# Optimization experiments

Measured on AMD Instinct MI355X. Metric: run time of the kernel, lower is better.

The kernel has to match this reference:

```python
import jax, jax.numpy as jnp
import numpy as np
import math

D_MODEL = 1024
D_INNER = 2048
N_HEADS = 8
D_STATE = 64
D_CONV = 4
CHUNK = 64
HEAD_DIM = D_INNER // N_HEADS
EPS = 1.1920929e-07  # torch RMSNorm default eps = finfo(fp32).eps


def _rms(x, g):
    return x * jax.lax.rsqrt(jnp.mean(x * x, axis=-1, keepdims=True) + EPS) * g


def setup_inputs() -> dict:
    key = jax.random.key(0)
    ks = jax.random.split(key, 8)
    B, S = 32, 256
    proj_out = 2 * D_INNER + 2 * N_HEADS * D_STATE + N_HEADS  # 5128
    s = 0.02
    lambdas = [0.999, 0.995, 0.99, 0.98, 0.95, 0.9, 0.8, 0.7]
    A_log = jnp.log(jnp.asarray([-math.log(l) for l in lambdas], jnp.float32))
    return {
        "hidden": jax.random.normal(ks[0], (B, S, D_MODEL), jnp.float32),
        "W_in": jax.random.normal(ks[1], (proj_out, D_MODEL), jnp.float32) * s,
        "conv_w": jax.random.normal(ks[2], (D_INNER, 1, D_CONV), jnp.float32) * 0.2,
        "conv_b": jax.random.normal(ks[3], (D_INNER,), jnp.float32) * 0.02,
        "W_dt": jax.random.normal(ks[4], (D_INNER, N_HEADS), jnp.float32) * 0.1,
        "b_dt": jax.random.normal(ks[5], (D_INNER,), jnp.float32) * 0.1,
        "A_log": A_log,
        "D": jnp.ones((N_HEADS,), jnp.float32),
        "W_out": jax.random.normal(ks[6], (D_MODEL, D_INNER), jnp.float32) * s,
        "g_in": jnp.ones((D_MODEL,), jnp.float32),
        "g_out": jnp.ones((D_INNER,), jnp.float32),
    }


def reference(hidden, W_in, conv_w, conv_b, W_dt, b_dt, A_log, D, W_out, g_in, g_out):
    B, S, _ = hidden.shape
    residual = hidden
    h = _rms(hidden, g_in)
    proj = h @ W_in.T  # [B,S,5128]
    o1, o2 = D_INNER, 2 * D_INNER
    o3 = o2 + N_HEADS * D_STATE
    o4 = o3 + N_HEADS * D_STATE
    z = proj[..., :o1]
    x = proj[..., o1:o2]
    Bf = proj[..., o2:o3]
    Cf = proj[..., o3:o4]
    dt_raw = proj[..., o4:]
    # causal depthwise conv1d (pad left d_conv-1, trim to S)
    xt = jnp.transpose(x, (0, 2, 1))  # [B, d_inner, S]
    xc = jax.lax.conv_general_dilated(
        xt, conv_w, (1,), [(D_CONV - 1, 0)],
        feature_group_count=D_INNER, dimension_numbers=("NCH", "OIH", "NCH"))
    x = jax.nn.silu(jnp.transpose(xc + conv_b[None, :, None], (0, 2, 1)))
    # dt: project 8 -> d_inner then mean over head_dim -> per-head dt
    dt = dt_raw @ W_dt.T + b_dt  # [B,S,d_inner]
    dt_h = jax.nn.softplus(dt.reshape(B, S, N_HEADS, HEAD_DIM).mean(-1))  # non-TTT path (S<384)
    Bs = Bf.reshape(B, S, N_HEADS, D_STATE)
    Cs = Cf.reshape(B, S, N_HEADS, D_STATE)
    x_h = x.reshape(B, S, N_HEADS, HEAD_DIM)
    # chunked SSD scan
    A = -jnp.exp(A_log)  # [H]
    nC, L = S // CHUNK, CHUNK
    xck = x_h.reshape(B, nC, L, N_HEADS, HEAD_DIM)
    Bck = Bs.reshape(B, nC, L, N_HEADS, D_STATE)
    Cck = Cs.reshape(B, nC, L, N_HEADS, D_STATE)
    logA = dt_h.reshape(B, nC, L, N_HEADS) * A  # [B,c,L,H]
    lcs = jnp.cumsum(logA, axis=2)
    lcs_t = jnp.transpose(lcs, (0, 1, 3, 2))  # [B,c,H,L]
    tril = jnp.tril(jnp.ones((L, L), bool))
    M = jnp.where(tril, jnp.exp(lcs_t[..., :, None] - lcs_t[..., None, :]), 0.0)  # [B,c,H,L,L]
    # intra-chunk: sum_{s<=l,n} C[l,n] M[l,s] B[s,n] x[s,d]
    G = jnp.einsum("bclhn,bcshn->bchls", Cck, Bck)
    intra = jnp.einsum("bchls,bcshd->bclhd", G * M, xck)
    # per-chunk state contributions and decays
    Mlast = jnp.exp(lcs_t[..., -1:] - lcs_t)  # [B,c,H,L] decay from step s to chunk end
    states = jnp.einsum("bchs,bcshn,bcshd->bchdn", Mlast, Bck, xck)  # [B,c,H,hD,N]
    tdec = jnp.exp(lcs[:, :, -1, :])  # [B,c,H]
    def step(hst, inp):
        td, st = inp
        return td[..., None, None] * hst + st, hst
    init = jnp.zeros((B, N_HEADS, HEAD_DIM, D_STATE), x.dtype)
    _, h0 = jax.lax.scan(step, init, (jnp.moveaxis(tdec, 1, 0), jnp.moveaxis(states, 1, 0)))
    # inter-chunk: decay(l) * C[l] . h_start
    inter = jnp.exp(lcs)[..., None] * jnp.einsum("bclhn,cbhdn->bclhd", Cck, h0)
    y = (intra + inter).reshape(B, S, N_HEADS, HEAD_DIM) + x_h * D[None, None, :, None]
    y = y.reshape(B, S, D_INNER) * jax.nn.silu(z)
    y = _rms(y, g_out)
    return residual + y @ W_out.T
```

## Files before the change

kernel.cpp:

```cpp
#include <hip/hip_runtime.h>
#include <hip/hip_bf16.h>
#include <math.h>

typedef __hip_bfloat16 bf16;
typedef __attribute__((ext_vector_type(8))) short short8;
typedef __attribute__((ext_vector_type(4))) float f32x4;

#define AS1 __attribute__((address_space(1)))
#define AS3 __attribute__((address_space(3)))

#define D_MODEL 1024
#define D_INNER 2048
#define N_HEADS 8
#define D_STATE 64
#define CHUNK 64
#define HEAD_DIM 256
#define NCHUNK 4
#define BATCH 32
#define SEQ 256
#define ROWS (BATCH*SEQ)
#define PROJ_N 5128
#define PROJ_NPAD 5248
#define O1 D_INNER
#define O2 (2*D_INNER)
#define O3 (O2 + N_HEADS*D_STATE)
#define O4 (O3 + N_HEADS*D_STATE)
#define EPSF 1.1920929e-07f

__device__ __forceinline__ float silu_f(float x){ return x / (1.0f + expf(-x)); }
__device__ __forceinline__ float b2f(bf16 v){ return __bfloat162float(v); }
__device__ __forceinline__ bf16  f2b(float v){ return __float2bfloat16(v); }
__device__ __forceinline__ short f2s(float v){ bf16 b = __float2bfloat16(v); union{bf16 b; short s;} u; u.b=b; return u.s; }
__device__ __forceinline__ float s2f(short v){ union{short s; bf16 b;} u; u.s=v; return __bfloat162float(u.b); }

__device__ __forceinline__ void gl16(const void* g, void* l){
    __builtin_amdgcn_global_load_lds((const AS1 void*)g, (AS3 void*)l, 16, 0, 0);
}

__device__ __forceinline__ float block_sum_256(float v){
    __shared__ float sm[4];
    #pragma unroll
    for (int o = 32; o > 0; o >>= 1) v += __shfl_down(v, o, 64);
    int lane = threadIdx.x & 63, w = threadIdx.x >> 6;
    if (lane == 0) sm[w] = v;
    __syncthreads();
    return sm[0] + sm[1] + sm[2] + sm[3];
}

__global__ __launch_bounds__(256) void k_rms_in(const float* __restrict__ x,
                                                const float* __restrict__ g,
                                                bf16* __restrict__ out){
    int row = blockIdx.x, t = threadIdx.x;
    const float4* xr = (const float4*)(x + (size_t)row * D_MODEL);
    float4 v = xr[t];
    float ss = v.x*v.x + v.y*v.y + v.z*v.z + v.w*v.w;
    ss = block_sum_256(ss);
    float sc = rsqrtf(ss * (1.0f/(float)D_MODEL) + EPSF);
    float4 gv = ((const float4*)g)[t];
    union { ushort4 u; bf16 b[4]; } o;
    o.b[0] = f2b(v.x*sc*gv.x); o.b[1] = f2b(v.y*sc*gv.y);
    o.b[2] = f2b(v.z*sc*gv.z); o.b[3] = f2b(v.w*sc*gv.w);
    ((ushort4*)(out + (size_t)row * D_MODEL))[t] = o.u;
}

__global__ __launch_bounds__(256) void k_cvt_pad(const float* __restrict__ in,
                                                 bf16* __restrict__ out,
                                                 int n_in, int n_out){
    int i = (blockIdx.x * 256 + threadIdx.x) * 4;
    if (i >= n_out) return;
    union { ushort4 u; bf16 b[4]; } o;
    if (i + 3 < n_in){
        float4 v = *(const float4*)(in + i);
        o.b[0]=f2b(v.x); o.b[1]=f2b(v.y); o.b[2]=f2b(v.z); o.b[3]=f2b(v.w);
    } else {
        #pragma unroll
        for (int j = 0; j < 4; j++) o.b[j] = f2b((i+j < n_in) ? in[i+j] : 0.f);
    }
    *(ushort4*)(out + i) = o.u;
}


__device__ __forceinline__ short8 ld32(const short* base, int row, int g){
    int sr = row >> 1;
    int e8 = (((row & 1) << 2) | g) ^ (sr & 7);
    return *(const short8*)(base + sr*64 + e8*8);
}

__device__ __forceinline__ void stage_j(const bf16* __restrict__ Ag,
                                        const bf16* __restrict__ Bg,
                                        int K, size_t bm, size_t bn, int t,
                                        short* buf, int j){
    const int tid = threadIdx.x;
    const int wid = tid >> 6;
    int cidx = j*256 + tid;
    int srow = cidx >> 3, s8 = cidx & 7;
    int eff = s8 ^ (srow & 7);
    int grow = srow*2 + (eff >> 2);
    int gcol = t*32 + (eff & 3)*8;
    const bf16* src = (grow < 128)
        ? Ag + (bm + grow) * (size_t)K + gcol
        : Bg + (bn + grow - 128) * (size_t)K + gcol;
    gl16(src, buf + (size_t)(j*256 + wid*64)*8);
}

__device__ __forceinline__ void gemm_ring3(const bf16* __restrict__ Ag,
                                           const bf16* __restrict__ Bg,
                                           int K, size_t bm, size_t bn,
                                           short* lds, f32x4 (&acc)[4][4]){
    constexpr int TILE = 256*32;
    const int NT = K >> 5;
    const int lane = threadIdx.x & 63;
    const int wid = threadIdx.x >> 6;
    const int wm = wid >> 1, wn = wid & 1;
    const int fr = lane & 15, g = lane >> 4;

    #pragma unroll
    for (int j = 0; j < 4; j++) stage_j(Ag, Bg, K, bm, bn, 0, lds, j);
    #pragma unroll
    for (int j = 0; j < 4; j++) stage_j(Ag, Bg, K, bm, bn, 1, lds + TILE, j);
    asm volatile("s_waitcnt vmcnt(4)" ::: "memory");
    __builtin_amdgcn_sched_barrier(0);
    __builtin_amdgcn_s_barrier();
    __builtin_amdgcn_sched_barrier(0);

    int cur = 0;
    for (int t = 0; t < NT; t++){
        short* buf = lds + cur*TILE;
        int stgi = cur + 2; if (stgi >= 3) stgi -= 3;
        short* stg = lds + stgi*TILE;
        short8 a[4], b[4];
        #pragma unroll
        for (int m = 0; m < 4; m++) a[m] = ld32(buf, wm*64 + m*16 + fr, g);
        #pragma unroll
        for (int n = 0; n < 4; n++) b[n] = ld32(buf, 128 + wn*64 + n*16 + fr, g);
        if (t + 2 < NT){
            #pragma unroll
            for (int j = 0; j < 4; j++) stage_j(Ag, Bg, K, bm, bn, t+2, stg, j);
        }
        __builtin_amdgcn_s_setprio(1);
        #pragma unroll
        for (int m = 0; m < 4; m++)
            #pragma unroll
            for (int n = 0; n < 4; n++)
                acc[m][n] = __builtin_amdgcn_mfma_f32_16x16x32_bf16(a[m], b[n], acc[m][n], 0, 0, 0);
        __builtin_amdgcn_s_setprio(0);
        __builtin_amdgcn_sched_barrier(0);
        if (t + 2 < NT)      asm volatile("s_waitcnt vmcnt(4)" ::: "memory");
        else if (t + 1 < NT) asm volatile("s_waitcnt vmcnt(0)" ::: "memory");
        __builtin_amdgcn_sched_barrier(0);
        __builtin_amdgcn_s_barrier();
        __builtin_amdgcn_sched_barrier(0);
        cur = cur + 1 == 3 ? 0 : cur + 1;
    }
}

__global__ __launch_bounds__(256, 3) void k_gemm1_r3(const bf16* __restrict__ A,
                                                     const bf16* __restrict__ B,
                                                     bf16* __restrict__ z,
                                                     bf16* __restrict__ xp,
                                                     bf16* __restrict__ Bc,
                                                     bf16* __restrict__ Cc,
                                                     float* __restrict__ dtr){
    extern __shared__ short lds[];
    int wg = (blockIdx.x & 7)*328 + (blockIdx.x >> 3);
    size_t bm = (size_t)(wg / 41) * 128;
    size_t bn = (size_t)(wg % 41) * 128;
    f32x4 acc[4][4] = {};
    gemm_ring3(A, B, D_MODEL, bm, bn, lds, acc);
    const int lane = threadIdx.x & 63;
    const int wid = threadIdx.x >> 6;
    const int wm = wid >> 1, wn = wid & 1;
    int cr = (lane >> 4)*4, cc = lane & 15;
    #pragma unroll
    for (int m = 0; m < 4; m++){
        size_t r0 = bm + wm*64 + m*16 + cr;
        #pragma unroll
        for (int n = 0; n < 4; n++){
            int c = (int)bn + wn*64 + n*16 + cc;
            #pragma unroll
            for (int j = 0; j < 4; j++){
                float v = acc[m][n][j];
                size_t r = r0 + j;
                if (c < O1)            z  [r * D_INNER + c]        = f2b(v);
                else if (c < O2)       xp [r * D_INNER + (c - O1)] = f2b(v);
                else if (c < O3)       Bc [r * 512 + (c - O2)]     = f2b(v);
                else if (c < O4)       Cc [r * 512 + (c - O3)]     = f2b(v);
                else if (c < PROJ_N)   dtr[r * 8 + (c - O4)]       = v;
            }
        }
    }
}

__global__ __launch_bounds__(256, 3) void k_gemm2_r3(const bf16* __restrict__ A,
                                                     const bf16* __restrict__ B,
                                                     const float* __restrict__ res,
                                                     float* __restrict__ C){
    extern __shared__ short lds[];
    int wg = (blockIdx.x & 7)*64 + (blockIdx.x >> 3);
    size_t bm = (size_t)(wg >> 3) * 128;
    size_t bn = (size_t)(wg & 7) * 128;
    f32x4 acc[4][4] = {};
    gemm_ring3(A, B, D_INNER, bm, bn, lds, acc);
    const int lane = threadIdx.x & 63;
    const int wid = threadIdx.x >> 6;
    const int wm = wid >> 1, wn = wid & 1;
    int cr = (lane >> 4)*4, cc = lane & 15;
    #pragma unroll
    for (int m = 0; m < 4; m++){
        size_t r0 = bm + wm*64 + m*16 + cr;
        #pragma unroll
        for (int n = 0; n < 4; n++){
            size_t c = bn + wn*64 + n*16 + cc;
            #pragma unroll
            for (int j = 0; j < 4; j++){
                size_t r = r0 + j;
                C[r * D_MODEL + c] = acc[m][n][j] + res[r * D_MODEL + c];
            }
        }
    }
}

__global__ __launch_bounds__(256) void k_conv_silu(const bf16* __restrict__ xp,
                                                   const float* __restrict__ cw,
                                                   const float* __restrict__ cb,
                                                   bf16* __restrict__ xout){
    int b = blockIdx.x;
    int c = blockIdx.y * 256 + threadIdx.x;
    float w0 = cw[c*4+0], w1 = cw[c*4+1], w2 = cw[c*4+2], w3 = cw[c*4+3];
    float bias = cb[c];
    const bf16* ib = xp + (size_t)b * SEQ * D_INNER + c;
    bf16* ob = xout + (size_t)b * SEQ * D_INNER + c;
    float x0 = 0.f, x1 = 0.f, x2 = 0.f;
    for (int s = 0; s < SEQ; s++){
        float x3 = b2f(ib[(size_t)s * D_INNER]);
        float a = x0*w0 + x1*w1 + x2*w2 + x3*w3 + bias;
        ob[(size_t)s * D_INNER] = f2b(silu_f(a));
        x0 = x1; x1 = x2; x2 = x3;
    }
}

__global__ __launch_bounds__(64) void k_prep(const float* __restrict__ W_dt,
                                             const float* __restrict__ b_dt,
                                             const float* __restrict__ A_log,
                                             float* __restrict__ misc){
    int t = threadIdx.x;
    int h = t >> 3, k = t & 7;
    float s = 0.f;
    for (int d = 0; d < HEAD_DIM; d++) s += W_dt[(size_t)(h*HEAD_DIM + d) * N_HEADS + k];
    misc[t] = s * (1.0f/(float)HEAD_DIM);
    if (t < 8){
        float sb = 0.f;
        for (int d = 0; d < HEAD_DIM; d++) sb += b_dt[t*HEAD_DIM + d];
        misc[64 + t] = sb * (1.0f/(float)HEAD_DIM);
        misc[72 + t] = -expf(A_log[t]);
    }
}

__global__ __launch_bounds__(64) void k_dt_lcs(const float* __restrict__ dtr,
                                               const float* __restrict__ misc,
                                               float* __restrict__ lcs,
                                               float* __restrict__ tdec){
    __shared__ float sm[80];
    __shared__ float la[CHUNK][N_HEADS];
    int bc = blockIdx.x;
    int l = threadIdx.x;
    for (int i = l; i < 80; i += 64) sm[i] = misc[i];
    __syncthreads();
    const float* dr = dtr + (size_t)(bc*CHUNK + l) * 8;
    float d0 = dr[0], d1 = dr[1], d2 = dr[2], d3 = dr[3];
    float d4 = dr[4], d5 = dr[5], d6 = dr[6], d7 = dr[7];
    #pragma unroll
    for (int h = 0; h < 8; h++){
        float dt = sm[64+h]
                 + d0*sm[h*8+0] + d1*sm[h*8+1] + d2*sm[h*8+2] + d3*sm[h*8+3]
                 + d4*sm[h*8+4] + d5*sm[h*8+5] + d6*sm[h*8+6] + d7*sm[h*8+7];
        float sp = (dt > 20.f) ? dt : log1pf(expf(dt));
        la[l][h] = sp * sm[72+h];
    }
    __syncthreads();
    float out[8];
    #pragma unroll
    for (int h = 0; h < 8; h++) out[h] = 0.f;
    for (int l2 = 0; l2 <= l; l2++){
        #pragma unroll
        for (int h = 0; h < 8; h++) out[h] += la[l2][h];
    }
    float* lo = lcs + (size_t)(bc*CHUNK + l) * N_HEADS;
    #pragma unroll
    for (int h = 0; h < 8; h++) lo[h] = out[h];
    if (l == 63){
        #pragma unroll
        for (int h = 0; h < 8; h++) tdec[bc*N_HEADS + h] = expf(out[h]);
    }
}

#define LB   0
#define LC   4096
#define LGM  8192
#define LXT  12800
#define LSH  29184
#define LF   45568
#define LDS_BYTES 91904

__device__ __forceinline__ short8 frag_sw(const short* arr, int r, int k){
    return *(const short8*)(arr + r*64 + (k ^ ((r&7)<<3)));
}

__global__ __launch_bounds__(256, 1) void k_ssm(const bf16* __restrict__ Bc,
                                                const bf16* __restrict__ Cc,
                                                bf16* xg,
                                                const float* __restrict__ lcs,
                                                const float* __restrict__ tdec,
                                                const float* __restrict__ Dv){
    extern __shared__ short lds[];
    short* Blds  = lds + LB;
    short* Clds  = lds + LC;
    short* GMlds = lds + LGM;
    short* XTlds = lds + LXT;
    short* Shr   = lds + LSH;
    float* el = (float*)(lds + LF);
    float* ml = el + 64;
    float* ee = el + 128;

    const int tid = threadIdx.x;
    const int lane = tid & 63;
    const int wid = tid >> 6;
    const int fr = lane & 15;
    const int fk = (lane >> 4) * 8;
    const int r0 = (lane >> 4) * 4;
    const int b = blockIdx.x >> 3, h = blockIdx.x & 7;
    const float Dh = Dv[h];

    f32x4 carry[4][4] = {};

    for (int c = 0; c < NCHUNK; c++){
        const int bc = b*NCHUNK + c;
        __syncthreads();
        #pragma unroll
        for (int i = 0; i < 2; i++){
            int slot = i*256 + tid;
            int s = slot >> 3, u = slot & 7;
            size_t rb = (size_t)(bc*CHUNK + s) * 512 + h*64 + ((u ^ (s&7)) * 8);
            gl16(Bc + rb, Blds + slot*8);
            gl16(Cc + rb, Clds + slot*8);
        }
        #pragma unroll
        for (int i = 0; i < 8; i++){
            int slot = i*256 + tid;
            int s = slot >> 5, ck = slot & 31;
            gl16(xg + (size_t)(bc*CHUNK + s) * D_INNER + h*HEAD_DIM + ck*8, Shr + slot*8);
        }
        if (tid < 64) el[tid] = lcs[(size_t)(bc*CHUNK + tid) * N_HEADS + h];
        __syncthreads();
        if (tid < 64){
            float e63 = el[63];
            ml[tid] = expf(e63 - el[tid]);
            ee[tid] = expf(el[tid]);
        }
        #pragma unroll
        for (int i = 0; i < 8; i++){
            short8 t8;
            #pragma unroll
            for (int j = 0; j < 8; j++) t8[j] = Shr[(i*8 + j)*HEAD_DIM + tid];
            *(short8*)(XTlds + tid*64 + ((i*8) ^ ((tid&7)<<3))) = t8;
        }
        __syncthreads();
        {
            f32x4 accg[4] = {};
            #pragma unroll
            for (int kk = 0; kk < 2; kk++){
                short8 a = frag_sw(Clds, wid*16 + fr, kk*32 + fk);
                #pragma unroll
                for (int nt = 0; nt < 4; nt++){
                    short8 bb = frag_sw(Blds, nt*16 + fr, kk*32 + fk);
                    accg[nt] = __builtin_amdgcn_mfma_f32_16x16x32_bf16(a, bb, accg[nt], 0, 0, 0);
                }
            }
            #pragma unroll
            for (int nt = 0; nt < 4; nt++){
                int s = nt*16 + fr;
                float els = el[s];
                #pragma unroll
                for (int j = 0; j < 4; j++){
                    int l = wid*16 + r0 + j;
                    float f = (s <= l) ? expf(el[l] - els) : 0.f;
                    GMlds[l*72 + s] = f2s(accg[nt][j] * f);
                }
            }
            int crow = wid*16 + (lane >> 2), cq = lane & 3;
            float fe = ee[crow];
            #pragma unroll
            for (int half = 0; half < 2; half++){
                short8 v = *(short8*)(Clds + crow*64 + cq*16 + half*8);
                #pragma unroll
                for (int j = 0; j < 8; j++) v[j] = f2s(s2f(v[j]) * fe);
                *(short8*)(Clds + crow*64 + cq*16 + half*8) = v;
            }
        }
        #pragma unroll
        for (int mt = 0; mt < 4; mt++)
            #pragma unroll
            for (int nt = 0; nt < 4; nt++)
                #pragma unroll
                for (int j = 0; j < 4; j++){
                    int d = wid*64 + mt*16 + r0 + j;
                    int n = nt*16 + fr;
                    Shr[d*64 + (n ^ ((d&7)<<3))] = f2s(carry[mt][nt][j]);
                }
        float btv[16];
        {
            int bn_ = tid & 63, bq = tid >> 6;
            #pragma unroll
            for (int i = 0; i < 16; i++){
                int s = bq*16 + i;
                btv[i] = s2f(Blds[s*64 + (bn_ ^ ((s&7)<<3))]) * ml[s];
            }
        }
        __syncthreads();
        {
            int bn_ = tid & 63, bq = tid >> 6;
            #pragma unroll
            for (int i = 0; i < 16; i++){
                int s = bq*16 + i;
                Blds[bn_*64 + (s ^ ((bn_&7)<<3))] = f2s(btv[i]);
            }
        }
        {
            f32x4 accy[4][4] = {};
            #pragma unroll
            for (int kk = 0; kk < 2; kk++){
                short8 ag[4], ae[4], bx[4], bh[4];
                #pragma unroll
                for (int mt = 0; mt < 4; mt++){
                    ag[mt] = *(const short8*)(GMlds + (mt*16 + fr)*72 + kk*32 + fk);
                    ae[mt] = frag_sw(Clds, mt*16 + fr, kk*32 + fk);
                }
                #pragma unroll
                for (int nt = 0; nt < 4; nt++){
                    int d = wid*64 + nt*16 + fr;
                    bx[nt] = frag_sw(XTlds, d, kk*32 + fk);
                    bh[nt] = frag_sw(Shr,  d, kk*32 + fk);
                }
                #pragma unroll
                for (int mt = 0; mt < 4; mt++)
                    #pragma unroll
                    for (int nt = 0; nt < 4; nt++){
                        accy[mt][nt] = __builtin_amdgcn_mfma_f32_16x16x32_bf16(ag[mt], bx[nt], accy[mt][nt], 0, 0, 0);
                        accy[mt][nt] = __builtin_amdgcn_mfma_f32_16x16x32_bf16(ae[mt], bh[nt], accy[mt][nt], 0, 0, 0);
                    }
            }
            #pragma unroll
            for (int mt = 0; mt < 4; mt++)
                #pragma unroll
                for (int nt = 0; nt < 4; nt++){
                    int d = wid*64 + nt*16 + fr;
                    #pragma unroll
                    for (int j = 0; j < 4; j++){
                        int l = mt*16 + r0 + j;
                        float xv = s2f(XTlds[d*64 + (l ^ ((d&7)<<3))]);
                        xg[(size_t)(bc*CHUNK + l) * D_INNER + h*HEAD_DIM + d] = f2b(accy[mt][nt][j] + xv*Dh);
                    }
                }
        }
        __syncthreads();
        {
            f32x4 accs[4][4] = {};
            #pragma unroll
            for (int kk = 0; kk < 2; kk++){
                short8 ax[4], bt[4];
                #pragma unroll
                for (int mt = 0; mt < 4; mt++)
                    ax[mt] = frag_sw(XTlds, wid*64 + mt*16 + fr, kk*32 + fk);
                #pragma unroll
                for (int nt = 0; nt < 4; nt++)
                    bt[nt] = frag_sw(Blds, nt*16 + fr, kk*32 + fk);
                #pragma unroll
                for (int mt = 0; mt < 4; mt++)
                    #pragma unroll
                    for (int nt = 0; nt < 4; nt++)
                        accs[mt][nt] = __builtin_amdgcn_mfma_f32_16x16x32_bf16(ax[mt], bt[nt], accs[mt][nt], 0, 0, 0);
            }
            float td = tdec[bc*N_HEADS + h];
            #pragma unroll
            for (int mt = 0; mt < 4; mt++)
                #pragma unroll
                for (int nt = 0; nt < 4; nt++)
                    carry[mt][nt] = td * carry[mt][nt] + accs[mt][nt];
        }
    }
}

__global__ __launch_bounds__(256) void k_gate_rms(const bf16* __restrict__ y,
                                                  const bf16* __restrict__ z,
                                                  const float* __restrict__ g,
                                                  bf16* __restrict__ yn){
    int row = blockIdx.x, t = threadIdx.x;
    union { uint4 u; bf16 b[8]; } yv, zv, ov;
    yv.u = ((const uint4*)(y + (size_t)row * D_INNER))[t];
    zv.u = ((const uint4*)(z + (size_t)row * D_INNER))[t];
    float v[8];
    float ss = 0.f;
    #pragma unroll
    for (int i = 0; i < 8; i++){
        float a = b2f(yv.b[i]);
        float q = b2f(zv.b[i]);
        v[i] = a * silu_f(q);
        ss += v[i]*v[i];
    }
    ss = block_sum_256(ss);
    float sc = rsqrtf(ss * (1.0f/(float)D_INNER) + EPSF);
    const float4* g4 = (const float4*)g;
    float4 ga = g4[2*t], gb = g4[2*t+1];
    float gg[8] = {ga.x,ga.y,ga.z,ga.w,gb.x,gb.y,gb.z,gb.w};
    #pragma unroll
    for (int i = 0; i < 8; i++) ov.b[i] = f2b(v[i]*sc*gg[i]);
    ((uint4*)(yn + (size_t)row * D_INNER))[t] = ov.u;
}

extern "C" void kernel_launch(void* const* d_in, const int* in_sizes, int n_in,
                              void* d_out, int out_size, void* d_ws, size_t ws_size,
                              hipStream_t stream){
    const float* hidden = (const float*)d_in[0];
    const float* W_in   = (const float*)d_in[1];
    const float* conv_w = (const float*)d_in[2];
    const float* conv_b = (const float*)d_in[3];
    const float* W_dt   = (const float*)d_in[4];
    const float* b_dt   = (const float*)d_in[5];
    const float* A_log  = (const float*)d_in[6];
    const float* Dv     = (const float*)d_in[7];
    const float* W_out  = (const float*)d_in[8];
    const float* g_in   = (const float*)d_in[9];
    const float* g_out  = (const float*)d_in[10];

    char* ws = (char*)d_ws;
    bf16*  z    = (bf16*)(ws + 0);
    bf16*  xp   = (bf16*)(ws + 33554432);
    bf16*  x    = (bf16*)(ws + 67108864);
    bf16*  Bc   = (bf16*)(ws + 100663296);
    bf16*  Cc   = (bf16*)(ws + 109051904);
    float* dtr  = (float*)(ws + 117440512);
    float* lcs  = (float*)(ws + 117702656);
    float* tdec = (float*)(ws + 117964800);
    float* misc = (float*)(ws + 117968896);
    bf16*  Wb   = (bf16*)(ws + 117969408);
    bf16*  hnb  = (bf16*)(ws + 128979456);
    bf16*  yn   = xp;

    k_rms_in<<<ROWS, 256, 0, stream>>>(hidden, g_in, hnb);
    k_cvt_pad<<<(PROJ_NPAD*D_MODEL/4 + 255)/256, 256, 0, stream>>>(W_in, Wb, PROJ_N*D_MODEL, PROJ_NPAD*D_MODEL);
    hipFuncSetAttribute((const void*)k_gemm1_r3, hipFuncAttributeMaxDynamicSharedMemorySize, 49152);
    k_gemm1_r3<<<(ROWS/128)*(PROJ_NPAD/128), 256, 49152, stream>>>(hnb, Wb, z, xp, Bc, Cc, dtr);
    k_conv_silu<<<dim3(BATCH, D_INNER/256), 256, 0, stream>>>(xp, conv_w, conv_b, x);
    k_prep<<<1, 64, 0, stream>>>(W_dt, b_dt, A_log, misc);
    k_dt_lcs<<<BATCH*NCHUNK, 64, 0, stream>>>(dtr, misc, lcs, tdec);
    hipFuncSetAttribute((const void*)k_ssm, hipFuncAttributeMaxDynamicSharedMemorySize, LDS_BYTES);
    k_ssm<<<BATCH*N_HEADS, 256, LDS_BYTES, stream>>>(Bc, Cc, x, lcs, tdec, Dv);
    k_gate_rms<<<ROWS, 256, 0, stream>>>(x, z, g_out, yn);
    k_cvt_pad<<<(D_MODEL*D_INNER/4 + 255)/256, 256, 0, stream>>>(W_out, Wb, D_MODEL*D_INNER, D_MODEL*D_INNER);
    hipFuncSetAttribute((const void*)k_gemm2_r3, hipFuncAttributeMaxDynamicSharedMemorySize, 49152);
    k_gemm2_r3<<<(ROWS/128)*(D_MODEL/128), 256, 49152, stream>>>(yn, Wb, hidden, (float*)d_out);
}
```

Baseline: 309.6 us.

## Enlarge GEMM tiles to 512-thread blocks with four-stage LDS ring

Both projection GEMMs now run 512-thread workgroups with larger tiles: 256x256 for the input projection and 128x256 for the output projection. The LDS ring grows from three to four stages, prefetching three tiles ahead. The MFMA loop is split into two halves so B fragment loads and global prefetches interleave with compute. Larger tiles raise arithmetic intensity and cut redundant global traffic. The cost is more LDS and registers per block, lower occupancy, and extra padding columns from PROJ_NPAD 5376.

After: 345.8 us. 1.12x slower.

```diff
diff --git a/kernel.cpp b/kernel.cpp
--- a/kernel.cpp
+++ b/kernel.cpp
@@ -20,7 +20,7 @@
 #define SEQ 256
 #define ROWS (BATCH*SEQ)
 #define PROJ_N 5128
-#define PROJ_NPAD 5248
+#define PROJ_NPAD 5376
 #define O1 D_INNER
 #define O2 (2*D_INNER)
 #define O3 (O2 + N_HEADS*D_STATE)
@@ -86,94 +86,162 @@
     return *(const short8*)(base + sr*64 + e8*8);
 }
 
-__device__ __forceinline__ void stage_j(const bf16* __restrict__ Ag,
+template<int AROWS>
+__device__ __forceinline__ void stage_u(const bf16* __restrict__ Ag,
                                         const bf16* __restrict__ Bg,
                                         int K, size_t bm, size_t bn, int t,
                                         short* buf, int j){
     const int tid = threadIdx.x;
     const int wid = tid >> 6;
-    int cidx = j*256 + tid;
+    int cidx = j*512 + tid;
     int srow = cidx >> 3, s8 = cidx & 7;
     int eff = s8 ^ (srow & 7);
     int grow = srow*2 + (eff >> 2);
     int gcol = t*32 + (eff & 3)*8;
-    const bf16* src = (grow < 128)
+    const bf16* src = (grow < AROWS)
         ? Ag + (bm + grow) * (size_t)K + gcol
-        : Bg + (bn + grow - 128) * (size_t)K + gcol;
-    gl16(src, buf + (size_t)(j*256 + wid*64)*8);
-}
-
-__device__ __forceinline__ void gemm_ring3(const bf16* __restrict__ Ag,
+        : Bg + (bn + grow - AROWS) * (size_t)K + gcol;
+    gl16(src, buf + (size_t)(j*512 + wid*64)*8);
+}
+
+#define MFMA_BF16(A_,B_,C_) __builtin_amdgcn_mfma_f32_16x16x32_bf16(A_,B_,C_,0,0,0)
+
+__device__ __forceinline__ void gemm1_main(const bf16* __restrict__ Ag,
                                            const bf16* __restrict__ Bg,
-                                           int K, size_t bm, size_t bn,
-                                           short* lds, f32x4 (&acc)[4][4]){
-    constexpr int TILE = 256*32;
-    const int NT = K >> 5;
+                                           size_t bm, size_t bn,
+                                           short* lds, f32x4 (&acc)[8][4]){
+    constexpr int K = D_MODEL, NT = K/32, TILE = 512*32;
     const int lane = threadIdx.x & 63;
     const int wid = threadIdx.x >> 6;
-    const int wm = wid >> 1, wn = wid & 1;
+    const int wm = wid >> 2, wn = wid & 3;
     const int fr = lane & 15, g = lane >> 4;
-
-    #pragma unroll
-    for (int j = 0; j < 4; j++) stage_j(Ag, Bg, K, bm, bn, 0, lds, j);
-    #pragma unroll
-    for (int j = 0; j < 4; j++) stage_j(Ag, Bg, K, bm, bn, 1, lds + TILE, j);
-    asm volatile("s_waitcnt vmcnt(4)" ::: "memory");
+    #pragma unroll
+    for (int p = 0; p < 3; p++)
+        #pragma unroll
+        for (int j = 0; j < 4; j++) stage_u<256>(Ag, Bg, K, bm, bn, p, lds + p*TILE, j);
+    asm volatile("s_waitcnt vmcnt(8)" ::: "memory");
     __builtin_amdgcn_sched_barrier(0);
     __builtin_amdgcn_s_barrier();
     __builtin_amdgcn_sched_barrier(0);
-
     int cur = 0;
     for (int t = 0; t < NT; t++){
         short* buf = lds + cur*TILE;
-        int stgi = cur + 2; if (stgi >= 3) stgi -= 3;
-        short* stg = lds + stgi*TILE;
-        short8 a[4], b[4];
-        #pragma unroll
-        for (int m = 0; m < 4; m++) a[m] = ld32(buf, wm*64 + m*16 + fr, g);
-        #pragma unroll
-        for (int n = 0; n < 4; n++) b[n] = ld32(buf, 128 + wn*64 + n*16 + fr, g);
-        if (t + 2 < NT){
-            #pragma unroll
-            for (int j = 0; j < 4; j++) stage_j(Ag, Bg, K, bm, bn, t+2, stg, j);
-        }
+        int sg = cur + 3; if (sg >= 4) sg -= 4;
+        short* stg = lds + sg*TILE;
+        const bool ds = (t + 3 < NT);
+        short8 a[8], b[4];
+        #pragma unroll
+        for (int m = 0; m < 8; m++) a[m] = ld32(buf, wm*128 + m*16 + fr, g);
+        b[0] = ld32(buf, 256 + wn*64 +  0 + fr, g);
+        b[1] = ld32(buf, 256 + wn*64 + 16 + fr, g);
+        if (ds){ stage_u<256>(Ag,Bg,K,bm,bn,t+3,stg,0); stage_u<256>(Ag,Bg,K,bm,bn,t+3,stg,1); }
         __builtin_amdgcn_s_setprio(1);
         #pragma unroll
-        for (int m = 0; m < 4; m++)
-            #pragma unroll
-            for (int n = 0; n < 4; n++)
-                acc[m][n] = __builtin_amdgcn_mfma_f32_16x16x32_bf16(a[m], b[n], acc[m][n], 0, 0, 0);
+        for (int m = 0; m < 8; m++){
+            acc[m][0] = MFMA_BF16(a[m], b[0], acc[m][0]);
+            acc[m][1] = MFMA_BF16(a[m], b[1], acc[m][1]);
+        }
         __builtin_amdgcn_s_setprio(0);
         __builtin_amdgcn_sched_barrier(0);
-        if (t + 2 < NT)      asm volatile("s_waitcnt vmcnt(4)" ::: "memory");
+        b[2] = ld32(buf, 256 + wn*64 + 32 + fr, g);
+        b[3] = ld32(buf, 256 + wn*64 + 48 + fr, g);
+        if (ds){ stage_u<256>(Ag,Bg,K,bm,bn,t+3,stg,2); stage_u<256>(Ag,Bg,K,bm,bn,t+3,stg,3); }
+        __builtin_amdgcn_s_setprio(1);
+        #pragma unroll
+        for (int m = 0; m < 8; m++){
+            acc[m][2] = MFMA_BF16(a[m], b[2], acc[m][2]);
+            acc[m][3] = MFMA_BF16(a[m], b[3], acc[m][3]);
+        }
+        __builtin_amdgcn_s_setprio(0);
+        __builtin_amdgcn_sched_barrier(0);
+        if (t + 3 < NT)      asm volatile("s_waitcnt vmcnt(8)" ::: "memory");
+        else if (t + 2 < NT) asm volatile("s_waitcnt vmcnt(4)" ::: "memory");
         else if (t + 1 < NT) asm volatile("s_waitcnt vmcnt(0)" ::: "memory");
         __builtin_amdgcn_sched_barrier(0);
         __builtin_amdgcn_s_barrier();
         __builtin_amdgcn_sched_barrier(0);
-        cur = cur + 1 == 3 ? 0 : cur + 1;
-    }
-}
-
-__global__ __launch_bounds__(256, 3) void k_gemm1_r3(const bf16* __restrict__ A,
-                                                     const bf16* __restrict__ B,
-                                                     bf16* __restrict__ z,
-                                                     bf16* __restrict__ xp,
-                                                     bf16* __restrict__ Bc,
-                                                     bf16* __restrict__ Cc,
-                                                     float* __restrict__ dtr){
-    extern __shared__ short lds[];
-    int wg = (blockIdx.x & 7)*328 + (blockIdx.x >> 3);
-    size_t bm = (size_t)(wg / 41) * 128;
-    size_t bn = (size_t)(wg % 41) * 128;
-    f32x4 acc[4][4] = {};
-    gemm_ring3(A, B, D_MODEL, bm, bn, lds, acc);
+        cur = cur + 1 == 4 ? 0 : cur + 1;
+    }
+}
+
+__device__ __forceinline__ void gemm2_main(const bf16* __restrict__ Ag,
+                                           const bf16* __restrict__ Bg,
+                                           size_t bm, size_t bn,
+                                           short* lds, f32x4 (&acc)[4][4]){
+    constexpr int K = D_INNER, NT = K/32, TILE = 384*32;
     const int lane = threadIdx.x & 63;
     const int wid = threadIdx.x >> 6;
-    const int wm = wid >> 1, wn = wid & 1;
+    const int wm = wid >> 2, wn = wid & 3;
+    const int fr = lane & 15, g = lane >> 4;
+    #pragma unroll
+    for (int p = 0; p < 3; p++)
+        #pragma unroll
+        for (int j = 0; j < 3; j++) stage_u<128>(Ag, Bg, K, bm, bn, p, lds + p*TILE, j);
+    asm volatile("s_waitcnt vmcnt(6)" ::: "memory");
+    __builtin_amdgcn_sched_barrier(0);
+    __builtin_amdgcn_s_barrier();
+    __builtin_amdgcn_sched_barrier(0);
+    int cur = 0;
+    for (int t = 0; t < NT; t++){
+        short* buf = lds + cur*TILE;
+        int sg = cur + 3; if (sg >= 4) sg -= 4;
+        short* stg = lds + sg*TILE;
+        const bool ds = (t + 3 < NT);
+        short8 a[4], b[4];
+        #pragma unroll
+        for (int m = 0; m < 4; m++) a[m] = ld32(buf, wm*64 + m*16 + fr, g);
+        b[0] = ld32(buf, 128 + wn*64 +  0 + fr, g);
+        b[1] = ld32(buf, 128 + wn*64 + 16 + fr, g);
+        if (ds){ stage_u<128>(Ag,Bg,K,bm,bn,t+3,stg,0); stage_u<128>(Ag,Bg,K,bm,bn,t+3,stg,1); }
+        __builtin_amdgcn_s_setprio(1);
+        #pragma unroll
+        for (int m = 0; m < 4; m++){
+            acc[m][0] = MFMA_BF16(a[m], b[0], acc[m][0]);
+            acc[m][1] = MFMA_BF16(a[m], b[1], acc[m][1]);
+        }
+        __builtin_amdgcn_s_setprio(0);
+        __builtin_amdgcn_sched_barrier(0);
+        b[2] = ld32(buf, 128 + wn*64 + 32 + fr, g);
+        b[3] = ld32(buf, 128 + wn*64 + 48 + fr, g);
+        if (ds) stage_u<128>(Ag,Bg,K,bm,bn,t+3,stg,2);
+        __builtin_amdgcn_s_setprio(1);
+        #pragma unroll
+        for (int m = 0; m < 4; m++){
+            acc[m][2] = MFMA_BF16(a[m], b[2], acc[m][2]);
+            acc[m][3] = MFMA_BF16(a[m], b[3], acc[m][3]);
+        }
+        __builtin_amdgcn_s_setprio(0);
+        __builtin_amdgcn_sched_barrier(0);
+        if (t + 3 < NT)      asm volatile("s_waitcnt vmcnt(6)" ::: "memory");
+        else if (t + 2 < NT) asm volatile("s_waitcnt vmcnt(3)" ::: "memory");
+        else if (t + 1 < NT) asm volatile("s_waitcnt vmcnt(0)" ::: "memory");
+        __builtin_amdgcn_sched_barrier(0);
+        __builtin_amdgcn_s_barrier();
+        __builtin_amdgcn_sched_barrier(0);
+        cur = cur + 1 == 4 ? 0 : cur + 1;
+    }
+}
+
+__global__ __launch_bounds__(512, 2) void k_gemm1_f(const bf16* __restrict__ A,
+                                                    const bf16* __restrict__ B,
+                                                    bf16* __restrict__ z,
+                                                    bf16* __restrict__ xp,
+                                                    bf16* __restrict__ Bc,
+                                                    bf16* __restrict__ Cc,
+                                                    float* __restrict__ dtr){
+    extern __shared__ short lds[];
+    int wg = (blockIdx.x & 7)*84 + (blockIdx.x >> 3);
+    size_t bm = (size_t)(wg / 21) * 256;
+    size_t bn = (size_t)(wg % 21) * 256;
+    f32x4 acc[8][4] = {};
+    gemm1_main(A, B, bm, bn, lds, acc);
+    const int lane = threadIdx.x & 63;
+    const int wid = threadIdx.x >> 6;
+    const int wm = wid >> 2, wn = wid & 3;
     int cr = (lane >> 4)*4, cc = lane & 15;
     #pragma unroll
-    for (int m = 0; m < 4; m++){
-        size_t r0 = bm + wm*64 + m*16 + cr;
+    for (int m = 0; m < 8; m++){
+        size_t r0 = bm + wm*128 + m*16 + cr;
         #pragma unroll
         for (int n = 0; n < 4; n++){
             int c = (int)bn + wn*64 + n*16 + cc;
@@ -191,19 +259,19 @@
     }
 }
 
-__global__ __launch_bounds__(256, 3) void k_gemm2_r3(const bf16* __restrict__ A,
-                                                     const bf16* __restrict__ B,
-                                                     const float* __restrict__ res,
-                                                     float* __restrict__ C){
+__global__ __launch_bounds__(512, 2) void k_gemm2_f(const bf16* __restrict__ A,
+                                                    const bf16* __restrict__ B,
+                                                    const float* __restrict__ res,
+                                                    float* __restrict__ C){
     extern __shared__ short lds[];
-    int wg = (blockIdx.x & 7)*64 + (blockIdx.x >> 3);
-    size_t bm = (size_t)(wg >> 3) * 128;
-    size_t bn = (size_t)(wg & 7) * 128;
+    int wg = (blockIdx.x & 7)*32 + (blockIdx.x >> 3);
+    size_t bm = (size_t)(wg >> 2) * 128;
+    size_t bn = (size_t)(wg & 3) * 256;
     f32x4 acc[4][4] = {};
-    gemm_ring3(A, B, D_INNER, bm, bn, lds, acc);
+    gemm2_main(A, B, bm, bn, lds, acc);
     const int lane = threadIdx.x & 63;
     const int wid = threadIdx.x >> 6;
-    const int wm = wid >> 1, wn = wid & 1;
+    const int wm = wid >> 2, wn = wid & 3;
     int cr = (lane >> 4)*4, cc = lane & 15;
     #pragma unroll
     for (int m = 0; m < 4; m++){
@@ -548,8 +616,8 @@
 
     k_rms_in<<<ROWS, 256, 0, stream>>>(hidden, g_in, hnb);
     k_cvt_pad<<<(PROJ_NPAD*D_MODEL/4 + 255)/256, 256, 0, stream>>>(W_in, Wb, PROJ_N*D_MODEL, PROJ_NPAD*D_MODEL);
-    hipFuncSetAttribute((const void*)k_gemm1_r3, hipFuncAttributeMaxDynamicSharedMemorySize, 49152);
-    k_gemm1_r3<<<(ROWS/128)*(PROJ_NPAD/128), 256, 49152, stream>>>(hnb, Wb, z, xp, Bc, Cc, dtr);
+    hipFuncSetAttribute((const void*)k_gemm1_f, hipFuncAttributeMaxDynamicSharedMemorySize, 131072);
+    k_gemm1_f<<<(ROWS/256)*(PROJ_NPAD/256), 512, 131072, stream>>>(hnb, Wb, z, xp, Bc, Cc, dtr);
     k_conv_silu<<<dim3(BATCH, D_INNER/256), 256, 0, stream>>>(xp, conv_w, conv_b, x);
     k_prep<<<1, 64, 0, stream>>>(W_dt, b_dt, A_log, misc);
     k_dt_lcs<<<BATCH*NCHUNK, 64, 0, stream>>>(dtr, misc, lcs, tdec);
@@ -557,6 +625,6 @@
     k_ssm<<<BATCH*N_HEADS, 256, LDS_BYTES, stream>>>(Bc, Cc, x, lcs, tdec, Dv);
     k_gate_rms<<<ROWS, 256, 0, stream>>>(x, z, g_out, yn);
     k_cvt_pad<<<(D_MODEL*D_INNER/4 + 255)/256, 256, 0, stream>>>(W_out, Wb, D_MODEL*D_INNER, D_MODEL*D_INNER);
-    hipFuncSetAttribute((const void*)k_gemm2_r3, hipFuncAttributeMaxDynamicSharedMemorySize, 49152);
-    k_gemm2_r3<<<(ROWS/128)*(D_MODEL/128), 256, 49152, stream>>>(yn, Wb, hidden, (float*)d_out);
-}
+    hipFuncSetAttribute((const void*)k_gemm2_f, hipFuncAttributeMaxDynamicSharedMemorySize, 98304);
+    k_gemm2_f<<<(ROWS/128)*(D_MODEL/256), 512, 98304, stream>>>(yn, Wb, hidden, (float*)d_out);
+}
```

## Enlarge GEMM tiles to 256x128 with 8 waves and grouped tile ordering

Applied to the files above, without the earlier changes.

Both projection GEMMs move from 128x128 tiles on 256 threads to 256x128 tiles on 512 threads. Staging, the LDS ring and the wait counts are adjusted to the 384-row tile. The input-projection GEMM also gains a grouped block order of six N-tiles per group, with N padded to 5376, to improve L2 reuse of the weights. The aim is more reuse per loaded B tile and less total global traffic. The cost is more LDS per block, which may lower occupancy, plus some extra padded columns of work.

Result: faster. 287.6 us (-7.1%).

```diff
diff --git a/kernel.cpp b/kernel.cpp
--- a/kernel.cpp
+++ b/kernel.cpp
@@ -20,7 +20,7 @@
 #define SEQ 256
 #define ROWS (BATCH*SEQ)
 #define PROJ_N 5128
-#define PROJ_NPAD 5248
+#define PROJ_NPAD 5376
 #define O1 D_INNER
 #define O2 (2*D_INNER)
 #define O3 (O2 + N_HEADS*D_STATE)
@@ -86,28 +86,30 @@
     return *(const short8*)(base + sr*64 + e8*8);
 }
 
-__device__ __forceinline__ void stage_j(const bf16* __restrict__ Ag,
+__device__ __forceinline__ void stage_u(const bf16* __restrict__ Ag,
                                         const bf16* __restrict__ Bg,
                                         int K, size_t bm, size_t bn, int t,
                                         short* buf, int j){
     const int tid = threadIdx.x;
     const int wid = tid >> 6;
-    int cidx = j*256 + tid;
+    int cidx = j*512 + tid;
     int srow = cidx >> 3, s8 = cidx & 7;
     int eff = s8 ^ (srow & 7);
     int grow = srow*2 + (eff >> 2);
     int gcol = t*32 + (eff & 3)*8;
-    const bf16* src = (grow < 128)
+    const bf16* src = (grow < 256)
         ? Ag + (bm + grow) * (size_t)K + gcol
-        : Bg + (bn + grow - 128) * (size_t)K + gcol;
-    gl16(src, buf + (size_t)(j*256 + wid*64)*8);
-}
-
-__device__ __forceinline__ void gemm_ring3(const bf16* __restrict__ Ag,
-                                           const bf16* __restrict__ Bg,
-                                           int K, size_t bm, size_t bn,
-                                           short* lds, f32x4 (&acc)[4][4]){
-    constexpr int TILE = 256*32;
+        : Bg + (bn + grow - 256) * (size_t)K + gcol;
+    gl16(src, buf + (size_t)(j*512 + wid*64)*8);
+}
+
+#define MFMA_BF16(A_,B_,C_) __builtin_amdgcn_mfma_f32_16x16x32_bf16(A_,B_,C_,0,0,0)
+
+__device__ __forceinline__ void gemm_main(const bf16* __restrict__ Ag,
+                                          const bf16* __restrict__ Bg,
+                                          int K, size_t bm, size_t bn,
+                                          short* lds, f32x4 (&acc)[4][4]){
+    constexpr int TILE = 384*32;
     const int NT = K >> 5;
     const int lane = threadIdx.x & 63;
     const int wid = threadIdx.x >> 6;
@@ -115,10 +117,10 @@
     const int fr = lane & 15, g = lane >> 4;
 
     #pragma unroll
-    for (int j = 0; j < 4; j++) stage_j(Ag, Bg, K, bm, bn, 0, lds, j);
-    #pragma unroll
-    for (int j = 0; j < 4; j++) stage_j(Ag, Bg, K, bm, bn, 1, lds + TILE, j);
-    asm volatile("s_waitcnt vmcnt(4)" ::: "memory");
+    for (int j = 0; j < 3; j++) stage_u(Ag, Bg, K, bm, bn, 0, lds, j);
+    #pragma unroll
+    for (int j = 0; j < 3; j++) stage_u(Ag, Bg, K, bm, bn, 1, lds + TILE, j);
+    asm volatile("s_waitcnt vmcnt(3)" ::: "memory");
     __builtin_amdgcn_sched_barrier(0);
     __builtin_amdgcn_s_barrier();
     __builtin_amdgcn_sched_barrier(0);
@@ -126,26 +128,27 @@
     int cur = 0;
     for (int t = 0; t < NT; t++){
         short* buf = lds + cur*TILE;
-        int stgi = cur + 2; if (stgi >= 3) stgi -= 3;
-        short* stg = lds + stgi*TILE;
+        int sg = cur + 2; if (sg >= 3) sg -= 3;
+        short* stg = lds + sg*TILE;
         short8 a[4], b[4];
         #pragma unroll
         for (int m = 0; m < 4; m++) a[m] = ld32(buf, wm*64 + m*16 + fr, g);
         #pragma unroll
-        for (int n = 0; n < 4; n++) b[n] = ld32(buf, 128 + wn*64 + n*16 + fr, g);
+        for (int n = 0; n < 4; n++) b[n] = ld32(buf, 256 + wn*64 + n*16 + fr, g);
         if (t + 2 < NT){
-            #pragma unroll
-            for (int j = 0; j < 4; j++) stage_j(Ag, Bg, K, bm, bn, t+2, stg, j);
+            stage_u(Ag, Bg, K, bm, bn, t+2, stg, 0);
+            stage_u(Ag, Bg, K, bm, bn, t+2, stg, 1);
+            stage_u(Ag, Bg, K, bm, bn, t+2, stg, 2);
         }
         __builtin_amdgcn_s_setprio(1);
         #pragma unroll
         for (int m = 0; m < 4; m++)
             #pragma unroll
             for (int n = 0; n < 4; n++)
-                acc[m][n] = __builtin_amdgcn_mfma_f32_16x16x32_bf16(a[m], b[n], acc[m][n], 0, 0, 0);
+                acc[m][n] = MFMA_BF16(a[m], b[n], acc[m][n]);
         __builtin_amdgcn_s_setprio(0);
         __builtin_amdgcn_sched_barrier(0);
-        if (t + 2 < NT)      asm volatile("s_waitcnt vmcnt(4)" ::: "memory");
+        if (t + 2 < NT)      asm volatile("s_waitcnt vmcnt(3)" ::: "memory");
         else if (t + 1 < NT) asm volatile("s_waitcnt vmcnt(0)" ::: "memory");
         __builtin_amdgcn_sched_barrier(0);
         __builtin_amdgcn_s_barrier();
@@ -154,19 +157,22 @@
     }
 }
 
-__global__ __launch_bounds__(256, 3) void k_gemm1_r3(const bf16* __restrict__ A,
-                                                     const bf16* __restrict__ B,
-                                                     bf16* __restrict__ z,
-                                                     bf16* __restrict__ xp,
-                                                     bf16* __restrict__ Bc,
-                                                     bf16* __restrict__ Cc,
-                                                     float* __restrict__ dtr){
+__global__ __launch_bounds__(512, 4) void k_gemm1_g(const bf16* __restrict__ A,
+                                                    const bf16* __restrict__ B,
+                                                    bf16* __restrict__ z,
+                                                    bf16* __restrict__ xp,
+                                                    bf16* __restrict__ Bc,
+                                                    bf16* __restrict__ Cc,
+                                                    float* __restrict__ dtr){
     extern __shared__ short lds[];
-    int wg = (blockIdx.x & 7)*328 + (blockIdx.x >> 3);
-    size_t bm = (size_t)(wg / 41) * 128;
-    size_t bn = (size_t)(wg % 41) * 128;
+    int wg = (blockIdx.x & 7)*168 + (blockIdx.x >> 3);
+    int grp = wg / 192, rem = wg % 192;
+    int nt_ = grp*6 + rem % 6;
+    int mt_ = rem / 6;
+    size_t bm = (size_t)mt_ * 256;
+    size_t bn = (size_t)nt_ * 128;
     f32x4 acc[4][4] = {};
-    gemm_ring3(A, B, D_MODEL, bm, bn, lds, acc);
+    gemm_main(A, B, D_MODEL, bm, bn, lds, acc);
     const int lane = threadIdx.x & 63;
     const int wid = threadIdx.x >> 6;
     const int wm = wid >> 1, wn = wid & 1;
@@ -191,16 +197,16 @@
     }
 }
 
-__global__ __launch_bounds__(256, 3) void k_gemm2_r3(const bf16* __restrict__ A,
-                                                     const bf16* __restrict__ B,
-                                                     const float* __restrict__ res,
-                                                     float* __restrict__ C){
+__global__ __launch_bounds__(512, 4) void k_gemm2_g(const bf16* __restrict__ A,
+                                                    const bf16* __restrict__ B,
+                                                    const float* __restrict__ res,
+                                                    float* __restrict__ C){
     extern __shared__ short lds[];
-    int wg = (blockIdx.x & 7)*64 + (blockIdx.x >> 3);
-    size_t bm = (size_t)(wg >> 3) * 128;
+    int wg = (blockIdx.x & 7)*32 + (blockIdx.x >> 3);
+    size_t bm = (size_t)(wg >> 3) * 256;
     size_t bn = (size_t)(wg & 7) * 128;
     f32x4 acc[4][4] = {};
-    gemm_ring3(A, B, D_INNER, bm, bn, lds, acc);
+    gemm_main(A, B, D_INNER, bm, bn, lds, acc);
     const int lane = threadIdx.x & 63;
     const int wid = threadIdx.x >> 6;
     const int wm = wid >> 1, wn = wid & 1;
@@ -548,8 +554,8 @@
 
     k_rms_in<<<ROWS, 256, 0, stream>>>(hidden, g_in, hnb);
     k_cvt_pad<<<(PROJ_NPAD*D_MODEL/4 + 255)/256, 256, 0, stream>>>(W_in, Wb, PROJ_N*D_MODEL, PROJ_NPAD*D_MODEL);
-    hipFuncSetAttribute((const void*)k_gemm1_r3, hipFuncAttributeMaxDynamicSharedMemorySize, 49152);
-    k_gemm1_r3<<<(ROWS/128)*(PROJ_NPAD/128), 256, 49152, stream>>>(hnb, Wb, z, xp, Bc, Cc, dtr);
+    hipFuncSetAttribute((const void*)k_gemm1_g, hipFuncAttributeMaxDynamicSharedMemorySize, 73728);
+    k_gemm1_g<<<(ROWS/256)*(PROJ_NPAD/128), 512, 73728, stream>>>(hnb, Wb, z, xp, Bc, Cc, dtr);
     k_conv_silu<<<dim3(BATCH, D_INNER/256), 256, 0, stream>>>(xp, conv_w, conv_b, x);
     k_prep<<<1, 64, 0, stream>>>(W_dt, b_dt, A_log, misc);
     k_dt_lcs<<<BATCH*NCHUNK, 64, 0, stream>>>(dtr, misc, lcs, tdec);
@@ -557,6 +563,6 @@
     k_ssm<<<BATCH*N_HEADS, 256, LDS_BYTES, stream>>>(Bc, Cc, x, lcs, tdec, Dv);
     k_gate_rms<<<ROWS, 256, 0, stream>>>(x, z, g_out, yn);
     k_cvt_pad<<<(D_MODEL*D_INNER/4 + 255)/256, 256, 0, stream>>>(W_out, Wb, D_MODEL*D_INNER, D_MODEL*D_INNER);
-    hipFuncSetAttribute((const void*)k_gemm2_r3, hipFuncAttributeMaxDynamicSharedMemorySize, 49152);
-    k_gemm2_r3<<<(ROWS/128)*(D_MODEL/128), 256, 49152, stream>>>(yn, Wb, hidden, (float*)d_out);
-}
+    hipFuncSetAttribute((const void*)k_gemm2_g, hipFuncAttributeMaxDynamicSharedMemorySize, 73728);
+    k_gemm2_g<<<(ROWS/256)*(D_MODEL/128), 512, 73728, stream>>>(yn, Wb, hidden, (float*)d_out);
+}
```
